# Kernel optimization log

Measured on AMD Instinct MI355X. Metric: run time of the kernel, lower is better.

Reference implementation:

```python
import jax, jax.numpy as jnp
import numpy as np

DIM = 2048
N_EXPERTS = 8
TOP_K = 2


def setup_inputs() -> dict:
    key = jax.random.key(0)
    ks = jax.random.split(key, 5)
    x = jax.random.normal(ks[0], (4, 4096, DIM), dtype=jnp.float32)
    # Linear(dim, dim, bias=False) stores weight as [out, in]; y = x @ W.T
    W_up = jax.random.normal(ks[1], (DIM, DIM), dtype=jnp.float32) * (1.0 / np.sqrt(DIM))
    W_down = jax.random.normal(ks[2], (DIM, DIM), dtype=jnp.float32) * (1.0 / np.sqrt(DIM))
    W_gate = jax.random.normal(ks[3], (N_EXPERTS, DIM), dtype=jnp.float32) * (1.0 / np.sqrt(DIM))
    # expert_weight: nn.Parameter(torch.randn(dim, dim)), applied as x @ W_expert
    W_expert = jax.random.normal(ks[4], (DIM, DIM), dtype=jnp.float32) * (1.0 / np.sqrt(DIM))
    return {"x": x, "W_up": W_up, "W_down": W_down, "W_gate": W_gate, "W_expert": W_expert}


def reference(x, W_up, W_down, W_gate, W_expert):
    # Gating: logits [B,S,E], top-k routing
    logits = jnp.einsum("bsd,ed->bse", x, W_gate)
    routing_weights, selected_experts = jax.lax.top_k(logits, TOP_K)  # [B,S,K]
    # Shared expert MLP
    shared_out = jnp.einsum("bsd,od->bso", jax.nn.relu(jnp.einsum("bsd,od->bso", x, W_up)), W_down)
    # Mock MoE combine: all selected experts share a single weight matrix, so the
    # dispatch-compute-scatter collapses to a softmax-normalized weighted sum of the
    # same expert output per token (weights sum to 1 over k).
    rw = jax.nn.softmax(routing_weights, axis=-1)  # [B,S,K]
    expert_out = jnp.einsum("bsd,do->bso", x, W_expert)  # shared across selected experts
    moe_out = jnp.sum(rw, axis=-1, keepdims=True) * expert_out
    return shared_out + moe_out
```

## Files before the change

kernel.cpp:

```cpp
#include <hip/hip_runtime.h>
#include <hip/hip_bf16.h>
#include <stdint.h>


#define DIM 2048
#define MTOT 16384

typedef unsigned short u16;
typedef __bf16 bf16x8 __attribute__((ext_vector_type(8)));
typedef float f32x4 __attribute__((ext_vector_type(4)));

__device__ __forceinline__ u16 f2bf(float f) {
    union { float f; unsigned int u; } a; a.f = f;
    unsigned int u = a.u;
    unsigned int r = (u + 0x7fffu + ((u >> 16) & 1u)) >> 16;
    return (u16)r;
}

__device__ __forceinline__ bf16x8 frag_load(const void* p) {
    union { uint4 u; bf16x8 b; } x;
    x.u = *(const uint4*)p;
    return x.b;
}

__global__ void cvt_pack(const float* __restrict__ src, u16* __restrict__ dst,
                         long n4, int dld, int doff) {
    long i = (long)blockIdx.x * blockDim.x + threadIdx.x;
    long stride = (long)gridDim.x * blockDim.x;
    for (; i < n4; i += stride) {
        long e = i << 2;
        long row = e >> 11;
        int col = (int)(e & 2047);
        float4 v = *(const float4*)(src + e);
        union { u16 q[4]; uint2 d; } u;
        u.q[0] = f2bf(v.x); u.q[1] = f2bf(v.y);
        u.q[2] = f2bf(v.z); u.q[3] = f2bf(v.w);
        *(uint2*)(dst + row * (long)dld + doff + col) = u.d;
    }
}

__global__ void cvt_transpose(const float* __restrict__ W, u16* __restrict__ dst) {
    __shared__ float t[32][33];
    int bx = blockIdx.x & 63;
    int by = blockIdx.x >> 6;
    int x = threadIdx.x & 31, y = threadIdx.x >> 5;
    #pragma unroll
    for (int j = 0; j < 32; j += 8)
        t[y + j][x] = W[(size_t)(by * 32 + y + j) * 2048 + bx * 32 + x];
    __syncthreads();
    #pragma unroll
    for (int j = 0; j < 32; j += 8)
        dst[(size_t)(bx * 32 + y + j) * 4096 + 2048 + by * 32 + x] = f2bf(t[x][y + j]);
}

template <int MODE>
__global__ __launch_bounds__(512, 2)
void gemm256(const u16* __restrict__ A, const u16* __restrict__ B,
             void* __restrict__ Cptr, int lda, int ldb, int K) {
    __shared__ char lds[2][65536];

    const int tid  = threadIdx.x;
    const int lane = tid & 63;
    const int wv   = tid >> 6;
    const int wr   = wv >> 2;
    const int wc   = wv & 3;

    int bid = blockIdx.x;
    int cpx = gridDim.x >> 3;
    int swz = (bid & 7) * cpx + (bid >> 3);
    int tile_n = swz & 7;
    int tile_m = swz >> 3;

    const int rowA0 = tile_m * 256;
    const int rowB0 = tile_n * 256;

    const int r_sub = tid >> 3;
    const int c_src = ((tid & 7) ^ (r_sub & 7)) << 3;
    const u16* pAb = A + (size_t)(rowA0 + r_sub) * lda + c_src;
    const u16* pBb = B + (size_t)(rowB0 + r_sub) * ldb + c_src;

    f32x4 acc[2][2][4][2];
    #pragma unroll
    for (int a = 0; a < 2; ++a)
        #pragma unroll
        for (int b = 0; b < 2; ++b)
            #pragma unroll
            for (int m = 0; m < 4; ++m)
                #pragma unroll
                for (int n = 0; n < 2; ++n)
                    acc[a][b][m][n] = (f32x4){0.f, 0.f, 0.f, 0.f};

    bf16x8 av[4][2];
    bf16x8 bv[2][2];
    const int kA = (lane >> 4) << 4;

#define STAGE_A(H, KOFF, BUF) do {                                              \
    const u16* _s = pAb + (size_t)((H) * 128) * lda + (KOFF);                   \
    __builtin_amdgcn_global_load_lds(                                           \
        (const __attribute__((address_space(1))) void*)_s,                      \
        (__attribute__((address_space(3))) void*)((char*)lds[BUF] + (H)*16384 + (wv<<10)), \
        16, 0, 0);                                                              \
    __builtin_amdgcn_global_load_lds(                                           \
        (const __attribute__((address_space(1))) void*)(_s + (size_t)64 * lda), \
        (__attribute__((address_space(3))) void*)((char*)lds[BUF] + (H)*16384 + 8192 + (wv<<10)), \
        16, 0, 0);                                                              \
  } while (0)

#define STAGE_B(H, KOFF, BUF) do {                                              \
    const u16* _s = pBb + (size_t)((H) * 128) * ldb + (KOFF);                   \
    __builtin_amdgcn_global_load_lds(                                           \
        (const __attribute__((address_space(1))) void*)_s,                      \
        (__attribute__((address_space(3))) void*)((char*)lds[BUF] + 32768 + (H)*16384 + (wv<<10)), \
        16, 0, 0);                                                              \
    __builtin_amdgcn_global_load_lds(                                           \
        (const __attribute__((address_space(1))) void*)(_s + (size_t)64 * ldb), \
        (__attribute__((address_space(3))) void*)((char*)lds[BUF] + 32768 + (H)*16384 + 8192 + (wv<<10)), \
        16, 0, 0);                                                              \
  } while (0)

#define DSREAD_A(MH, CUR) do {                                                  \
    _Pragma("unroll")                                                           \
    for (int m = 0; m < 4; ++m) {                                               \
        int ra = (wr << 6) + (m << 4) + (lane & 15);                            \
        const char* _b = (const char*)lds[CUR] + (MH)*16384 + (ra << 7);        \
        int sw = (ra & 7) << 4;                                                 \
        av[m][0] = frag_load(_b + (kA ^ sw));                                   \
        av[m][1] = frag_load(_b + ((64 + kA) ^ sw));                            \
    } } while (0)

#define DSREAD_B(NH, CUR) do {                                                  \
    _Pragma("unroll")                                                           \
    for (int n = 0; n < 2; ++n) {                                               \
        int rb = (wc << 5) + (n << 4) + (lane & 15);                            \
        const char* _b = (const char*)lds[CUR] + 32768 + (NH)*16384 + (rb << 7);\
        int sw = (rb & 7) << 4;                                                 \
        bv[n][0] = frag_load(_b + (kA ^ sw));                                   \
        bv[n][1] = frag_load(_b + ((64 + kA) ^ sw));                            \
    } } while (0)

#define MFMA_Q(MH, NH) do {                                                     \
    __builtin_amdgcn_s_setprio(1);                                              \
    _Pragma("unroll")                                                           \
    for (int m = 0; m < 4; ++m)                                                 \
        _Pragma("unroll")                                                       \
        for (int n = 0; n < 2; ++n) {                                           \
            acc[MH][NH][m][n] = __builtin_amdgcn_mfma_f32_16x16x32_bf16(        \
                av[m][0], bv[n][0], acc[MH][NH][m][n], 0, 0, 0);                \
            acc[MH][NH][m][n] = __builtin_amdgcn_mfma_f32_16x16x32_bf16(        \
                av[m][1], bv[n][1], acc[MH][NH][m][n], 0, 0, 0);                \
        }                                                                       \
    __builtin_amdgcn_s_setprio(0);                                              \
  } while (0)

#define WAIT_VM(N) asm volatile("s_waitcnt vmcnt(" #N ")" ::: "memory")
#define WAIT_LGKM() do {                                                        \
    asm volatile("s_waitcnt lgkmcnt(0)" ::: "memory");                          \
    __builtin_amdgcn_sched_barrier(0);                                          \
  } while (0)
#define BAR() __builtin_amdgcn_s_barrier()

    STAGE_A(0, 0, 0);
    STAGE_B(0, 0, 0);
    STAGE_B(1, 0, 0);
    STAGE_A(1, 0, 0);
    WAIT_VM(4);
    BAR();

    const int nK = K >> 6;
    int cur = 0;
    for (int t = 0; t < nK - 1; ++t) {
        const int koff = (t + 1) << 6;
        const int nxt = cur ^ 1;
        DSREAD_A(0, cur); DSREAD_B(0, cur);
        STAGE_A(0, koff, nxt);
        WAIT_VM(4); BAR(); WAIT_LGKM();
        MFMA_Q(0, 0);
        BAR();
        DSREAD_B(1, cur);
        STAGE_B(0, koff, nxt);
        WAIT_VM(4); BAR(); WAIT_LGKM();
        MFMA_Q(0, 1);
        BAR();
        DSREAD_A(1, cur);
        STAGE_B(1, koff, nxt);
        WAIT_VM(6); BAR(); WAIT_LGKM();
        MFMA_Q(1, 1);
        BAR();
        DSREAD_B(0, cur);
        STAGE_A(1, koff, nxt);
        WAIT_VM(4); BAR(); WAIT_LGKM();
        MFMA_Q(1, 0);
        BAR();
        cur = nxt;
    }

    DSREAD_A(0, cur); DSREAD_B(0, cur);
    WAIT_VM(2); BAR(); WAIT_LGKM();
    MFMA_Q(0, 0);
    DSREAD_B(1, cur);
    WAIT_VM(0); BAR(); WAIT_LGKM();
    MFMA_Q(0, 1);
    DSREAD_A(1, cur);
    WAIT_LGKM();
    MFMA_Q(1, 1);
    DSREAD_B(0, cur);
    WAIT_LGKM();
    MFMA_Q(1, 0);

    #pragma unroll
    for (int mh = 0; mh < 2; ++mh)
        #pragma unroll
        for (int m = 0; m < 4; ++m)
            #pragma unroll
            for (int r = 0; r < 4; ++r) {
                int row = rowA0 + mh * 128 + (wr << 6) + (m << 4) + ((lane >> 4) << 2) + r;
                #pragma unroll
                for (int nh = 0; nh < 2; ++nh)
                    #pragma unroll
                    for (int n = 0; n < 2; ++n) {
                        int col = tile_n * 256 + nh * 128 + (wc << 5) + (n << 4) + (lane & 15);
                        float v = acc[mh][nh][m][n][r];
                        if (MODE == 0) {
                            ((u16*)Cptr)[(size_t)row * 4096 + col] = f2bf(fmaxf(v, 0.f));
                        } else {
                            ((float*)Cptr)[(size_t)row * 2048 + col] = v;
                        }
                    }
            }
#undef STAGE_A
#undef STAGE_B
#undef DSREAD_A
#undef DSREAD_B
#undef MFMA_Q
#undef WAIT_VM
#undef WAIT_LGKM
#undef BAR
}

extern "C" void kernel_launch(void* const* d_in, const int* in_sizes, int n_in,
                              void* d_out, int out_size, void* d_ws, size_t ws_size,
                              hipStream_t stream) {
    const float* x        = (const float*)d_in[0];
    const float* W_up     = (const float*)d_in[1];
    const float* W_down   = (const float*)d_in[2];
    const float* W_expert = (const float*)d_in[4];

    u16* Abig = (u16*)d_ws;
    u16* Bbig = Abig + (size_t)MTOT * 4096;
    u16* Wup  = Bbig + (size_t)DIM * 4096;

    cvt_pack<<<2048, 256, 0, stream>>>(x, Abig, (long)MTOT * DIM / 4, 4096, 2048);
    cvt_pack<<<1024, 256, 0, stream>>>(W_up, Wup, (long)DIM * DIM / 4, 2048, 0);
    cvt_pack<<<1024, 256, 0, stream>>>(W_down, Bbig, (long)DIM * DIM / 4, 4096, 0);
    cvt_transpose<<<4096, 256, 0, stream>>>(W_expert, Bbig);

    gemm256<0><<<512, 512, 0, stream>>>(Abig + 2048, Wup, Abig, 4096, 2048, 2048);
    gemm256<1><<<512, 512, 0, stream>>>(Abig, Bbig, d_out, 4096, 4096, 4096);
}
```

Baseline: 411.8 us.

## Merge GEMM main-loop quadrant phases into two halves with double B fragments

The main loop of the bf16 MFMA GEMM used four phases per K step, each with its own LDS fragment read, global-to-LDS stage, vmcnt/lgkmcnt wait and two barriers. It now runs two half-phases. Both B fragment sets are read into separate register arrays (bva/bvb) and reused across the two MFMA quadrants of each half, and the waits and a single barrier come after the MFMAs. This is meant to cut barrier and wait stalls and let LDS reads overlap with matrix math. In exchange it uses more VGPRs for the extra B fragments, and it drops the explicit sched_barrier, so instruction ordering is left to the compiler.

```diff
diff --git a/kernel.cpp b/kernel.cpp
--- a/kernel.cpp
+++ b/kernel.cpp
@@ -91,7 +91,8 @@
                     acc[a][b][m][n] = (f32x4){0.f, 0.f, 0.f, 0.f};
 
     bf16x8 av[4][2];
-    bf16x8 bv[2][2];
+    bf16x8 bva[2][2];
+    bf16x8 bvb[2][2];
     const int kA = (lane >> 4) << 4;
 
 #define STAGE_A(H, KOFF, BUF) do {                                              \
@@ -128,42 +129,39 @@
         av[m][1] = frag_load(_b + ((64 + kA) ^ sw));                            \
     } } while (0)
 
-#define DSREAD_B(NH, CUR) do {                                                  \
+#define DSREAD_B(NH, CUR, DST) do {                                             \
     _Pragma("unroll")                                                           \
     for (int n = 0; n < 2; ++n) {                                               \
         int rb = (wc << 5) + (n << 4) + (lane & 15);                            \
         const char* _b = (const char*)lds[CUR] + 32768 + (NH)*16384 + (rb << 7);\
         int sw = (rb & 7) << 4;                                                 \
-        bv[n][0] = frag_load(_b + (kA ^ sw));                                   \
-        bv[n][1] = frag_load(_b + ((64 + kA) ^ sw));                            \
+        DST[n][0] = frag_load(_b + (kA ^ sw));                                  \
+        DST[n][1] = frag_load(_b + ((64 + kA) ^ sw));                           \
     } } while (0)
 
-#define MFMA_Q(MH, NH) do {                                                     \
+#define MFMA_Q(MH, NH, BV) do {                                                 \
     __builtin_amdgcn_s_setprio(1);                                              \
     _Pragma("unroll")                                                           \
     for (int m = 0; m < 4; ++m)                                                 \
         _Pragma("unroll")                                                       \
         for (int n = 0; n < 2; ++n) {                                           \
             acc[MH][NH][m][n] = __builtin_amdgcn_mfma_f32_16x16x32_bf16(        \
-                av[m][0], bv[n][0], acc[MH][NH][m][n], 0, 0, 0);                \
+                av[m][0], BV[n][0], acc[MH][NH][m][n], 0, 0, 0);                \
             acc[MH][NH][m][n] = __builtin_amdgcn_mfma_f32_16x16x32_bf16(        \
-                av[m][1], bv[n][1], acc[MH][NH][m][n], 0, 0, 0);                \
+                av[m][1], BV[n][1], acc[MH][NH][m][n], 0, 0, 0);                \
         }                                                                       \
     __builtin_amdgcn_s_setprio(0);                                              \
   } while (0)
 
 #define WAIT_VM(N) asm volatile("s_waitcnt vmcnt(" #N ")" ::: "memory")
-#define WAIT_LGKM() do {                                                        \
-    asm volatile("s_waitcnt lgkmcnt(0)" ::: "memory");                          \
-    __builtin_amdgcn_sched_barrier(0);                                          \
-  } while (0)
+#define WAIT_LGKM0() asm volatile("s_waitcnt lgkmcnt(0)" ::: "memory")
 #define BAR() __builtin_amdgcn_s_barrier()
 
     STAGE_A(0, 0, 0);
     STAGE_B(0, 0, 0);
     STAGE_B(1, 0, 0);
     STAGE_A(1, 0, 0);
-    WAIT_VM(4);
+    WAIT_VM(2);
     BAR();
 
     const int nK = K >> 6;
@@ -171,41 +169,38 @@
     for (int t = 0; t < nK - 1; ++t) {
         const int koff = (t + 1) << 6;
         const int nxt = cur ^ 1;
-        DSREAD_A(0, cur); DSREAD_B(0, cur);
+        DSREAD_B(0, cur, bva);
+        DSREAD_B(1, cur, bvb);
+        DSREAD_A(0, cur);
         STAGE_A(0, koff, nxt);
-        WAIT_VM(4); BAR(); WAIT_LGKM();
-        MFMA_Q(0, 0);
-        BAR();
-        DSREAD_B(1, cur);
         STAGE_B(0, koff, nxt);
-        WAIT_VM(4); BAR(); WAIT_LGKM();
-        MFMA_Q(0, 1);
+        MFMA_Q(0, 0, bva);
+        MFMA_Q(0, 1, bvb);
+        WAIT_LGKM0();
+        WAIT_VM(4);
         BAR();
         DSREAD_A(1, cur);
         STAGE_B(1, koff, nxt);
-        WAIT_VM(6); BAR(); WAIT_LGKM();
-        MFMA_Q(1, 1);
-        BAR();
-        DSREAD_B(0, cur);
         STAGE_A(1, koff, nxt);
-        WAIT_VM(4); BAR(); WAIT_LGKM();
-        MFMA_Q(1, 0);
+        MFMA_Q(1, 1, bvb);
+        MFMA_Q(1, 0, bva);
+        WAIT_LGKM0();
+        WAIT_VM(2);
         BAR();
         cur = nxt;
     }
 
-    DSREAD_A(0, cur); DSREAD_B(0, cur);
-    WAIT_VM(2); BAR(); WAIT_LGKM();
-    MFMA_Q(0, 0);
-    DSREAD_B(1, cur);
-    WAIT_VM(0); BAR(); WAIT_LGKM();
-    MFMA_Q(0, 1);
+    DSREAD_B(0, cur, bva);
+    DSREAD_B(1, cur, bvb);
+    DSREAD_A(0, cur);
+    MFMA_Q(0, 0, bva);
+    MFMA_Q(0, 1, bvb);
+    WAIT_LGKM0();
+    WAIT_VM(0);
+    BAR();
     DSREAD_A(1, cur);
-    WAIT_LGKM();
-    MFMA_Q(1, 1);
-    DSREAD_B(0, cur);
-    WAIT_LGKM();
-    MFMA_Q(1, 0);
+    MFMA_Q(1, 1, bvb);
+    MFMA_Q(1, 0, bva);
 
     #pragma unroll
     for (int mh = 0; mh < 2; ++mh)
@@ -233,7 +228,7 @@
 #undef DSREAD_B
 #undef MFMA_Q
 #undef WAIT_VM
-#undef WAIT_LGKM
+#undef WAIT_LGKM0
 #undef BAR
 }
 
```

Measured after the change: 369.2 us. -10.3%, faster.
